# Kernel optimization log

Hardware: AMD Instinct MI355X
Metric: run time of the kernel (lower is better)

The kernel has to match this reference:

```python
import jax, jax.numpy as jnp
import numpy as np

B, S, HID = 32, 577, 768
NH, HD = 12, 64  # num heads, head dim (HID = NH*HD)


def setup_inputs() -> dict:
    key = jax.random.key(0)
    ks = jax.random.split(key, 8)
    scale = 1.0 / np.sqrt(HID)
    return {
        "hidden_states": jax.random.normal(ks[0], (B, S, HID), jnp.float32),
        "lateral_states": jax.random.normal(ks[1], (B, NH, S, HD), jnp.float32),
        "Wq": jax.random.normal(ks[2], (HID, HID), jnp.float32) * scale,
        "bq": jax.random.normal(ks[3], (HID,), jnp.float32) * 0.02,
        "Wk": jax.random.normal(ks[4], (HID, HID), jnp.float32) * scale,
        "bk": jax.random.normal(ks[5], (HID,), jnp.float32) * 0.02,
        "Wv": jax.random.normal(ks[6], (HID, HID), jnp.float32) * scale,
        "bv": jax.random.normal(ks[7], (HID,), jnp.float32) * 0.02,
        "mix_with": 0,  # 0 -> 'q', 1 -> 'k', 2 -> 'v'
    }


def _heads(x):
    # [B, S, HID] -> [B, NH, S, HD]
    return x.reshape(B, S, NH, HD).transpose(0, 2, 1, 3)


def reference(hidden_states, lateral_states, Wq, bq, Wk, bk, Wv, bv, mix_with):
    q = _heads(hidden_states @ Wq.T + bq)
    k = _heads(hidden_states @ Wk.T + bk)
    v = _heads(hidden_states @ Wv.T + bv)
    if mix_with == 0:
        q = q * lateral_states
    elif mix_with == 1:
        k = k * lateral_states
    elif mix_with == 2:
        v = v * lateral_states
    else:
        raise ValueError("mix_with must be 0 (q), 1 (k), or 2 (v)")
    scores = jnp.einsum("bhqd,bhkd->bhqk", q, k) / jnp.sqrt(jnp.float32(HD))
    probs = jax.nn.softmax(scores, axis=-1)
    ctx = jnp.einsum("bhqk,bhkd->bhqd", probs, v)
    # [B, NH, S, HD] -> [B, S, HID]
    return ctx.transpose(0, 2, 1, 3).reshape(B, S, HID)
```

## Files before the change

### kernel.cpp

```cpp
#include <hip/hip_runtime.h>

#define B_    32
#define S_    577
#define HID_  768
#define NH_   12
#define HD_   64
#define SPAD  640
#define SB_   5
#define MT_   160
#define KT_   12
#define NT_   18

typedef __attribute__((ext_vector_type(8))) short short8;
typedef __attribute__((ext_vector_type(4))) short short4s;
typedef __attribute__((ext_vector_type(4))) float float4_;

static __device__ __forceinline__ float bf2f(short s) {
    union { float f; unsigned u; } cvt;
    cvt.u = ((unsigned)(unsigned short)s) << 16;
    return cvt.f;
}
static __device__ __forceinline__ short f2bf(float f) {
    union { float f; unsigned u; } cvt;
    cvt.f = f;
    unsigned u = cvt.u;
    unsigned r = u + 0x7FFF + ((u >> 16) & 1);
    return (short)(r >> 16);
}

__global__ __launch_bounds__(256) void convA_kernel(
    const float* __restrict__ X, short* __restrict__ ximg)
{
    const int mt = blockIdx.x, kt = blockIdx.y;
    const int b = mt / SB_, sb = mt - b * SB_;
    short* img = ximg + ((size_t)mt * KT_ + kt) * 8192;
#pragma unroll
    for (int i = 0; i < 4; ++i) {
        const int j = i * 256 + threadIdx.x;
        const int row = j >> 3, kg = j & 7;
        const int s = sb * 128 + row;
        const int srow = (s < S_) ? s : 0;
        const float* src = X + ((size_t)b * S_ + srow) * HID_ + kt * 64 + kg * 8;
        float4_ f0 = *(const float4_*)src;
        float4_ f1 = *(const float4_*)(src + 4);
        short8 s8;
#pragma unroll
        for (int e = 0; e < 4; ++e) { s8[e] = f2bf(f0[e]); s8[e + 4] = f2bf(f1[e]); }
        *(short8*)(img + ((size_t)kg * 128 + row) * 8) = s8;
    }
}

__global__ __launch_bounds__(256) void convB_kernel(
    const float* __restrict__ Wq, const float* __restrict__ Wk,
    const float* __restrict__ Wv, short* __restrict__ wimg)
{
    const int nt = blockIdx.x, kt = blockIdx.y;
    const int z = nt / 6;
    const float* W = (z == 0) ? Wq : (z == 1) ? Wk : Wv;
    const int n0 = (nt - z * 6) * 128;
    short* img = wimg + ((size_t)nt * KT_ + kt) * 8192;
#pragma unroll
    for (int i = 0; i < 4; ++i) {
        const int j = i * 256 + threadIdx.x;
        const int row = j >> 3, kg = j & 7;
        const float* src = W + (size_t)(n0 + row) * HID_ + kt * 64 + kg * 8;
        float4_ f0 = *(const float4_*)src;
        float4_ f1 = *(const float4_*)(src + 4);
        short8 s8;
#pragma unroll
        for (int e = 0; e < 4; ++e) { s8[e] = f2bf(f0[e]); s8[e + 4] = f2bf(f1[e]); }
        *(short8*)(img + ((size_t)kg * 128 + row) * 8) = s8;
    }
}

__global__ __launch_bounds__(256) void gemm_kernel(
    const short* __restrict__ ximg, const short* __restrict__ wimg,
    const float* __restrict__ bq, const float* __restrict__ bk,
    const float* __restrict__ bv,
    const float* __restrict__ lat, const int* __restrict__ mixw,
    short* __restrict__ qo, short* __restrict__ ko, short* __restrict__ vo)
{
    __shared__ __align__(16) short eP[4][4608];

    const int bid0 = blockIdx.x;
    const int bids = (bid0 & 7) * 360 + (bid0 >> 3);
    const int mt = bids / NT_;
    const int nt = bids - mt * NT_;

    const int z   = nt / 6;
    const int nz0 = (nt - z * 6) * 128;
    const int b   = mt / SB_;
    const int s0  = (mt - b * SB_) * 128;

    const int tid  = threadIdx.x;
    const int wave = tid >> 6;
    const int lane = tid & 63;
    const int quad = lane >> 4;
    const int l16  = lane & 15;

    const short* ag = ximg + ((size_t)mt * KT_) * 8192;
    const short* bg = wimg + ((size_t)nt * KT_) * 8192;

    float4_ acc[4][4] = {};
    const int r0 = (wave & 1) * 64 + l16;
    const int c0 = (wave >> 1) * 64 + l16;

    for (int kt = 0; kt < KT_; ++kt) {
        const short* ak = ag + (size_t)kt * 8192;
        const short* bk8p = bg + (size_t)kt * 8192;
#pragma unroll
        for (int c = 0; c < 2; ++c) {
            const int kb = (c * 4 + quad) * 128;
            short8 af[4], bf4[4];
#pragma unroll
            for (int mi = 0; mi < 4; ++mi)
                af[mi] = *(const short8*)(ak + (kb + r0 + mi * 16) * 8);
#pragma unroll
            for (int g = 0; g < 4; ++g)
                bf4[g] = *(const short8*)(bk8p + (kb + c0 + g * 16) * 8);
            __builtin_amdgcn_s_setprio(1);
#pragma unroll
            for (int mi = 0; mi < 4; ++mi)
#pragma unroll
                for (int g = 0; g < 4; ++g)
                    acc[mi][g] = __builtin_amdgcn_mfma_f32_16x16x32_bf16(
                        af[mi], bf4[g], acc[mi][g], 0, 0, 0);
            __builtin_amdgcn_s_setprio(0);
        }
    }

    const int mwv = *mixw;
    const float* bb = (z == 0) ? bq : (z == 1) ? bk : bv;
    const int hh   = (nz0 + (wave >> 1) * 64) >> 6;
    const size_t bh = (size_t)b * NH_ + hh;
    const int sW   = s0 + (wave & 1) * 64;
    const int ch   = sW >> 6;
    short* P = eP[wave];

    if (z < 2) {
#pragma unroll
        for (int mi = 0; mi < 4; ++mi)
#pragma unroll
            for (int i = 0; i < 4; ++i) {
                const int ml = mi * 16 + quad * 4 + i;
                const int s  = sW + ml;
                const float* lp =
                    lat + (bh * S_ + (s < S_ ? s : S_ - 1)) * HD_;
#pragma unroll
                for (int g = 0; g < 4; ++g) {
                    const int d = g * 16 + l16;
                    float val = acc[mi][g][i] + bb[hh * 64 + d];
                    if (z == mwv) val *= lp[d];
                    P[ml * 72 + d] = f2bf(val);
                }
            }
    } else {
#pragma unroll
        for (int mi = 0; mi < 4; ++mi)
#pragma unroll
            for (int g = 0; g < 4; ++g) {
                const int d  = g * 16 + l16;
                const int mb = mi * 16 + quad * 4;
                short4s w;
#pragma unroll
                for (int i = 0; i < 4; ++i) {
                    const int s = sW + mb + i;
                    float val = acc[mi][g][i] + bb[hh * 64 + d];
                    if (mwv == 2)
                        val *= lat[(bh * S_ + (s < S_ ? s : S_ - 1)) * HD_ + d];
                    w[i] = f2bf(val);
                }
                *(short4s*)(P + d * 72 + mb) = w;
            }
    }

    const int rr = lane >> 3, cc = lane & 7;
    if (z == 0) {
        short* qb = qo + (size_t)bh * SPAD * HD_;
#pragma unroll
        for (int j = 0; j < 8; ++j) {
            const int r = j * 8 + rr;
            *(short8*)(qb + (size_t)(sW + r) * 64 + cc * 8) =
                *(const short8*)(P + r * 72 + cc * 8);
        }
    } else if (z == 1) {
        short* kb = ko + ((size_t)bh * 10 + ch) * 4096;
#pragma unroll
        for (int j = 0; j < 8; ++j) {
            const int r = j * 8 + rr;
            *(short8*)(kb + (cc * 64 + r) * 8) =
                *(const short8*)(P + r * 72 + cc * 8);
        }
    } else {
        short* vb = vo + ((size_t)bh * 10 + ch) * 4096;
#pragma unroll
        for (int j = 0; j < 8; ++j) {
            const int r = j * 8 + rr;
            *(short8*)(vb + (cc * 64 + r) * 8) =
                *(const short8*)(P + r * 72 + cc * 8);
        }
    }
}

__global__ __launch_bounds__(256) void attn_kernel(
    const short* __restrict__ q, const short* __restrict__ k,
    const short* __restrict__ vt, float* __restrict__ out)
{
    __shared__ __align__(16) short pbuf[4][16][64];

    const int bid0 = blockIdx.x;
    const int bids = (bid0 & 7) * 480 + (bid0 >> 3);
    const int bh = bids / 10;
    const int qt = bids - bh * 10;

    const int b    = bh / NH_;
    const int h    = bh - b * NH_;
    const int tid  = threadIdx.x;
    const int wave = tid >> 6;
    const int lane = tid & 63;
    const int quad = lane >> 4;
    const int l16  = lane & 15;
    const int q0   = qt * 64 + wave * 16;

    const short* qp   = q  + (size_t)bh * SPAD * HD_;
    const short* kimg = k  + (size_t)bh * 40960;
    const short* vimg = vt + (size_t)bh * 40960;

    const short8 aq0 = *(const short8*)(qp + (size_t)(q0 + l16) * HD_ + quad * 8);
    const short8 aq1 = *(const short8*)(qp + (size_t)(q0 + l16) * HD_ + 32 + quad * 8);

    float m_i[4], l_i[4];
    float4_ O[4] = {};
#pragma unroll
    for (int i = 0; i < 4; ++i) { m_i[i] = -3.0e38f; l_i[i] = 0.0f; }

    for (int kc = 0; kc < 10; ++kc) {
        const int key0 = kc * 64;
        const short* Kc = kimg + (size_t)kc * 4096;
        const short* Vc = vimg + (size_t)kc * 4096;

        float4_ sc[4] = {};
#pragma unroll
        for (int c = 0; c < 2; ++c) {
            const int kb = (c * 4 + quad) * 64;
            const short8 aq = c ? aq1 : aq0;
            short8 bk8[4];
#pragma unroll
            for (int g = 0; g < 4; ++g)
                bk8[g] = *(const short8*)(Kc + (kb + g * 16 + l16) * 8);
            __builtin_amdgcn_s_setprio(1);
#pragma unroll
            for (int g = 0; g < 4; ++g)
                sc[g] = __builtin_amdgcn_mfma_f32_16x16x32_bf16(aq, bk8[g], sc[g], 0, 0, 0);
            __builtin_amdgcn_s_setprio(0);
        }

        float kmask[4];
#pragma unroll
        for (int g = 0; g < 4; ++g)
            kmask[g] = (key0 + g * 16 + l16 < S_) ? 0.0f : -3.0e38f;

        float alpha[4];
#pragma unroll
        for (int i = 0; i < 4; ++i) {
            float s0 = sc[0][i] * 0.125f + kmask[0];
            float s1 = sc[1][i] * 0.125f + kmask[1];
            float s2 = sc[2][i] * 0.125f + kmask[2];
            float s3 = sc[3][i] * 0.125f + kmask[3];
            float cm = fmaxf(fmaxf(s0, s1), fmaxf(s2, s3));
#pragma unroll
            for (int off = 1; off < 16; off <<= 1)
                cm = fmaxf(cm, __shfl_xor(cm, off));
            const float mn = fmaxf(m_i[i], cm);
            alpha[i] = __expf(m_i[i] - mn);
            m_i[i] = mn;
            const short p0 = f2bf(__expf(s0 - mn));
            const short p1 = f2bf(__expf(s1 - mn));
            const short p2 = f2bf(__expf(s2 - mn));
            const short p3 = f2bf(__expf(s3 - mn));
            pbuf[wave][quad * 4 + i][l16]      = p0;
            pbuf[wave][quad * 4 + i][l16 + 16] = p1;
            pbuf[wave][quad * 4 + i][l16 + 32] = p2;
            pbuf[wave][quad * 4 + i][l16 + 48] = p3;
            float rs = (bf2f(p0) + bf2f(p1)) + (bf2f(p2) + bf2f(p3));
#pragma unroll
            for (int off = 1; off < 16; off <<= 1)
                rs += __shfl_xor(rs, off);
            l_i[i] = l_i[i] * alpha[i] + rs;
        }

#pragma unroll
        for (int g = 0; g < 4; ++g)
#pragma unroll
            for (int i = 0; i < 4; ++i) O[g][i] *= alpha[i];

#pragma unroll
        for (int c = 0; c < 2; ++c) {
            const short8 ap = *(const short8*)(&pbuf[wave][l16][c * 32 + quad * 8]);
            const int kb = (c * 4 + quad) * 64;
            short8 bv8[4];
#pragma unroll
            for (int g = 0; g < 4; ++g)
                bv8[g] = *(const short8*)(Vc + (kb + g * 16 + l16) * 8);
            __builtin_amdgcn_s_setprio(1);
#pragma unroll
            for (int g = 0; g < 4; ++g)
                O[g] = __builtin_amdgcn_mfma_f32_16x16x32_bf16(ap, bv8[g], O[g], 0, 0, 0);
            __builtin_amdgcn_s_setprio(0);
        }
    }

#pragma unroll
    for (int i = 0; i < 4; ++i) {
        const int s = q0 + quad * 4 + i;
        if (s >= S_) continue;
        const float inv = 1.0f / l_i[i];
#pragma unroll
        for (int g = 0; g < 4; ++g)
            out[((size_t)b * S_ + s) * HID_ + h * HD_ + g * 16 + l16] = O[g][i] * inv;
    }
}

extern "C" void kernel_launch(void* const* d_in, const int* in_sizes, int n_in,
                              void* d_out, int out_size, void* d_ws, size_t ws_size,
                              hipStream_t stream) {
    (void)in_sizes; (void)n_in; (void)out_size; (void)ws_size;

    const float* X   = (const float*)d_in[0];
    const float* lat = (const float*)d_in[1];
    const float* Wq  = (const float*)d_in[2];
    const float* bq  = (const float*)d_in[3];
    const float* Wk  = (const float*)d_in[4];
    const float* bk  = (const float*)d_in[5];
    const float* Wv  = (const float*)d_in[6];
    const float* bv  = (const float*)d_in[7];
    const int* mixw  = (const int*)d_in[8];
    float* out = (float*)d_out;

    const size_t per = (size_t)B_ * NH_ * SPAD * HD_;
    short* qw   = (short*)d_ws;
    short* kw   = qw + per;
    short* vw   = kw + per;
    short* wimg = vw + per;
    short* ximg = wimg + (size_t)NT_ * KT_ * 8192;

    convA_kernel<<<dim3(MT_, KT_), 256, 0, stream>>>(X, ximg);
    convB_kernel<<<dim3(NT_, KT_), 256, 0, stream>>>(Wq, Wk, Wv, wimg);
    gemm_kernel<<<dim3(NT_ * MT_), 256, 0, stream>>>(
        ximg, wimg, bq, bk, bv, lat, mixw, qw, kw, vw);
    attn_kernel<<<dim3(3840), 256, 0, stream>>>(qw, kw, vw, out);
}
```

Before: 406.5 us.

## Double per-block tile sizes in projection GEMM and attention kernels

The projection GEMM now has each block compute a 128x256 output tile, with each wave owning 64x128 and 32 accumulators, so A fragments are reused across twice as many columns. The attention kernel has each wave handle 32 query rows instead of 16, so every K and V fragment load feeds two MFMA row tiles. Grid sizes are halved to match. Both changes cut global and cache traffic per FLOP, but raise register pressure, which may lower occupancy, and leave fewer blocks for load balance.

```diff
diff --git a/kernel.cpp b/kernel.cpp
--- a/kernel.cpp
+++ b/kernel.cpp
@@ -83,12 +83,12 @@
     __shared__ __align__(16) short eP[4][4608];
 
     const int bid0 = blockIdx.x;
-    const int bids = (bid0 & 7) * 360 + (bid0 >> 3);
-    const int mt = bids / NT_;
-    const int nt = bids - mt * NT_;
-
-    const int z   = nt / 6;
-    const int nz0 = (nt - z * 6) * 128;
+    const int bids = (bid0 & 7) * 180 + (bid0 >> 3);
+    const int mt  = bids / 9;
+    const int nt9 = bids - mt * 9;
+
+    const int z   = nt9 / 3;
+    const int nb0 = (nt9 - z * 3) * 256;
     const int b   = mt / SB_;
     const int s0  = (mt - b * SB_) * 128;
 
@@ -97,13 +97,14 @@
     const int lane = tid & 63;
     const int quad = lane >> 4;
     const int l16  = lane & 15;
-
-    const short* ag = ximg + ((size_t)mt * KT_) * 8192;
-    const short* bg = wimg + ((size_t)nt * KT_) * 8192;
-
-    float4_ acc[4][4] = {};
-    const int r0 = (wave & 1) * 64 + l16;
-    const int c0 = (wave >> 1) * 64 + l16;
+    const int wr   = wave & 1;
+    const int wc   = wave >> 1;
+
+    const short* ag = ximg + (size_t)mt * KT_ * 8192;
+    const short* bg = wimg + (size_t)(z * 6 + (nb0 >> 7) + wc) * KT_ * 8192;
+
+    float4_ acc[4][8] = {};
+    const int r0 = wr * 64 + l16;
 
     for (int kt = 0; kt < KT_; ++kt) {
         const short* ak = ag + (size_t)kt * 8192;
@@ -111,93 +112,97 @@
 #pragma unroll
         for (int c = 0; c < 2; ++c) {
             const int kb = (c * 4 + quad) * 128;
-            short8 af[4], bf4[4];
+            short8 af[4], bf[8];
 #pragma unroll
             for (int mi = 0; mi < 4; ++mi)
                 af[mi] = *(const short8*)(ak + (kb + r0 + mi * 16) * 8);
 #pragma unroll
-            for (int g = 0; g < 4; ++g)
-                bf4[g] = *(const short8*)(bk8p + (kb + c0 + g * 16) * 8);
+            for (int g = 0; g < 8; ++g)
+                bf[g] = *(const short8*)(bk8p + (kb + g * 16 + l16) * 8);
             __builtin_amdgcn_s_setprio(1);
 #pragma unroll
             for (int mi = 0; mi < 4; ++mi)
 #pragma unroll
-                for (int g = 0; g < 4; ++g)
+                for (int g = 0; g < 8; ++g)
                     acc[mi][g] = __builtin_amdgcn_mfma_f32_16x16x32_bf16(
-                        af[mi], bf4[g], acc[mi][g], 0, 0, 0);
+                        af[mi], bf[g], acc[mi][g], 0, 0, 0);
             __builtin_amdgcn_s_setprio(0);
         }
     }
 
     const int mwv = *mixw;
     const float* bb = (z == 0) ? bq : (z == 1) ? bk : bv;
-    const int hh   = (nz0 + (wave >> 1) * 64) >> 6;
-    const size_t bh = (size_t)b * NH_ + hh;
-    const int sW   = s0 + (wave & 1) * 64;
-    const int ch   = sW >> 6;
+    const int sW = s0 + wr * 64;
+    const int ch = sW >> 6;
     short* P = eP[wave];
-
-    if (z < 2) {
-#pragma unroll
-        for (int mi = 0; mi < 4; ++mi)
-#pragma unroll
-            for (int i = 0; i < 4; ++i) {
-                const int ml = mi * 16 + quad * 4 + i;
-                const int s  = sW + ml;
-                const float* lp =
-                    lat + (bh * S_ + (s < S_ ? s : S_ - 1)) * HD_;
-#pragma unroll
-                for (int g = 0; g < 4; ++g) {
-                    const int d = g * 16 + l16;
-                    float val = acc[mi][g][i] + bb[hh * 64 + d];
-                    if (z == mwv) val *= lp[d];
-                    P[ml * 72 + d] = f2bf(val);
+    const int rr = lane >> 3, cc = lane & 7;
+
+#pragma unroll
+    for (int hs = 0; hs < 2; ++hs) {
+        const int hh = (nb0 >> 6) + wc * 2 + hs;
+        const size_t bh = (size_t)b * NH_ + hh;
+
+        if (z < 2) {
+#pragma unroll
+            for (int mi = 0; mi < 4; ++mi)
+#pragma unroll
+                for (int i = 0; i < 4; ++i) {
+                    const int ml = mi * 16 + quad * 4 + i;
+                    const int s  = sW + ml;
+                    const float* lp =
+                        lat + (bh * S_ + (s < S_ ? s : S_ - 1)) * HD_;
+#pragma unroll
+                    for (int gg = 0; gg < 4; ++gg) {
+                        const int d = gg * 16 + l16;
+                        float val = acc[mi][hs * 4 + gg][i] + bb[hh * 64 + d];
+                        if (z == mwv) val *= lp[d];
+                        P[ml * 72 + d] = f2bf(val);
+                    }
                 }
-            }
-    } else {
-#pragma unroll
-        for (int mi = 0; mi < 4; ++mi)
-#pragma unroll
-            for (int g = 0; g < 4; ++g) {
-                const int d  = g * 16 + l16;
-                const int mb = mi * 16 + quad * 4;
-                short4s w;
-#pragma unroll
-                for (int i = 0; i < 4; ++i) {
-                    const int s = sW + mb + i;
-                    float val = acc[mi][g][i] + bb[hh * 64 + d];
-                    if (mwv == 2)
-                        val *= lat[(bh * S_ + (s < S_ ? s : S_ - 1)) * HD_ + d];
-                    w[i] = f2bf(val);
+        } else {
+#pragma unroll
+            for (int mi = 0; mi < 4; ++mi)
+#pragma unroll
+                for (int gg = 0; gg < 4; ++gg) {
+                    const int d  = gg * 16 + l16;
+                    const int mb = mi * 16 + quad * 4;
+                    short4s w;
+#pragma unroll
+                    for (int i = 0; i < 4; ++i) {
+                        const int s = sW + mb + i;
+                        float val = acc[mi][hs * 4 + gg][i] + bb[hh * 64 + d];
+                        if (mwv == 2)
+                            val *= lat[(bh * S_ + (s < S_ ? s : S_ - 1)) * HD_ + d];
+                        w[i] = f2bf(val);
+                    }
+                    *(short4s*)(P + d * 72 + mb) = w;
                 }
-                *(short4s*)(P + d * 72 + mb) = w;
-            }
-    }
-
-    const int rr = lane >> 3, cc = lane & 7;
-    if (z == 0) {
-        short* qb = qo + (size_t)bh * SPAD * HD_;
-#pragma unroll
-        for (int j = 0; j < 8; ++j) {
-            const int r = j * 8 + rr;
-            *(short8*)(qb + (size_t)(sW + r) * 64 + cc * 8) =
-                *(const short8*)(P + r * 72 + cc * 8);
-        }
-    } else if (z == 1) {
-        short* kb = ko + ((size_t)bh * 10 + ch) * 4096;
-#pragma unroll
-        for (int j = 0; j < 8; ++j) {
-            const int r = j * 8 + rr;
-            *(short8*)(kb + (cc * 64 + r) * 8) =
-                *(const short8*)(P + r * 72 + cc * 8);
-        }
-    } else {
-        short* vb = vo + ((size_t)bh * 10 + ch) * 4096;
-#pragma unroll
-        for (int j = 0; j < 8; ++j) {
-            const int r = j * 8 + rr;
-            *(short8*)(vb + (cc * 64 + r) * 8) =
-                *(const short8*)(P + r * 72 + cc * 8);
+        }
+
+        if (z == 0) {
+            short* qb = qo + (size_t)bh * SPAD * HD_;
+#pragma unroll
+            for (int j = 0; j < 8; ++j) {
+                const int r = j * 8 + rr;
+                *(short8*)(qb + (size_t)(sW + r) * 64 + cc * 8) =
+                    *(const short8*)(P + r * 72 + cc * 8);
+            }
+        } else if (z == 1) {
+            short* kb_ = ko + ((size_t)bh * 10 + ch) * 4096;
+#pragma unroll
+            for (int j = 0; j < 8; ++j) {
+                const int r = j * 8 + rr;
+                *(short8*)(kb_ + (cc * 64 + r) * 8) =
+                    *(const short8*)(P + r * 72 + cc * 8);
+            }
+        } else {
+            short* vb = vo + ((size_t)bh * 10 + ch) * 4096;
+#pragma unroll
+            for (int j = 0; j < 8; ++j) {
+                const int r = j * 8 + rr;
+                *(short8*)(vb + (cc * 64 + r) * 8) =
+                    *(const short8*)(P + r * 72 + cc * 8);
+            }
         }
     }
 }
@@ -206,12 +211,12 @@
     const short* __restrict__ q, const short* __restrict__ k,
     const short* __restrict__ vt, float* __restrict__ out)
 {
-    __shared__ __align__(16) short pbuf[4][16][64];
+    __shared__ __align__(16) short pbuf[4][2][16][64];
 
     const int bid0 = blockIdx.x;
-    const int bids = (bid0 & 7) * 480 + (bid0 >> 3);
-    const int bh = bids / 10;
-    const int qt = bids - bh * 10;
+    const int bids = (bid0 & 7) * 240 + (bid0 >> 3);
+    const int bh = bids / 5;
+    const int qt = bids - bh * 5;
 
     const int b    = bh / NH_;
     const int h    = bh - b * NH_;
@@ -220,38 +225,47 @@
     const int lane = tid & 63;
     const int quad = lane >> 4;
     const int l16  = lane & 15;
-    const int q0   = qt * 64 + wave * 16;
+    const int q0   = qt * 128 + wave * 32;
 
     const short* qp   = q  + (size_t)bh * SPAD * HD_;
     const short* kimg = k  + (size_t)bh * 40960;
     const short* vimg = vt + (size_t)bh * 40960;
 
-    const short8 aq0 = *(const short8*)(qp + (size_t)(q0 + l16) * HD_ + quad * 8);
-    const short8 aq1 = *(const short8*)(qp + (size_t)(q0 + l16) * HD_ + 32 + quad * 8);
-
-    float m_i[4], l_i[4];
-    float4_ O[4] = {};
-#pragma unroll
-    for (int i = 0; i < 4; ++i) { m_i[i] = -3.0e38f; l_i[i] = 0.0f; }
+    short8 aq[2][2];
+#pragma unroll
+    for (int t = 0; t < 2; ++t)
+#pragma unroll
+        for (int c = 0; c < 2; ++c)
+            aq[t][c] = *(const short8*)(qp + (size_t)(q0 + t * 16 + l16) * HD_
+                                        + c * 32 + quad * 8);
+
+    float m_i[2][4], l_i[2][4];
+    float4_ O[2][4] = {};
+#pragma unroll
+    for (int t = 0; t < 2; ++t)
+#pragma unroll
+        for (int i = 0; i < 4; ++i) { m_i[t][i] = -3.0e38f; l_i[t][i] = 0.0f; }
 
     for (int kc = 0; kc < 10; ++kc) {
         const int key0 = kc * 64;
         const short* Kc = kimg + (size_t)kc * 4096;
         const short* Vc = vimg + (size_t)kc * 4096;
 
-        float4_ sc[4] = {};
+        float4_ sc[2][4] = {};
 #pragma unroll
         for (int c = 0; c < 2; ++c) {
             const int kb = (c * 4 + quad) * 64;
-            const short8 aq = c ? aq1 : aq0;
             short8 bk8[4];
 #pragma unroll
             for (int g = 0; g < 4; ++g)
                 bk8[g] = *(const short8*)(Kc + (kb + g * 16 + l16) * 8);
             __builtin_amdgcn_s_setprio(1);
 #pragma unroll
-            for (int g = 0; g < 4; ++g)
-                sc[g] = __builtin_amdgcn_mfma_f32_16x16x32_bf16(aq, bk8[g], sc[g], 0, 0, 0);
+            for (int t = 0; t < 2; ++t)
+#pragma unroll
+                for (int g = 0; g < 4; ++g)
+                    sc[t][g] = __builtin_amdgcn_mfma_f32_16x16x32_bf16(
+                        aq[t][c], bk8[g], sc[t][g], 0, 0, 0);
             __builtin_amdgcn_s_setprio(0);
         }
 
@@ -260,43 +274,46 @@
         for (int g = 0; g < 4; ++g)
             kmask[g] = (key0 + g * 16 + l16 < S_) ? 0.0f : -3.0e38f;
 
-        float alpha[4];
-#pragma unroll
-        for (int i = 0; i < 4; ++i) {
-            float s0 = sc[0][i] * 0.125f + kmask[0];
-            float s1 = sc[1][i] * 0.125f + kmask[1];
-            float s2 = sc[2][i] * 0.125f + kmask[2];
-            float s3 = sc[3][i] * 0.125f + kmask[3];
-            float cm = fmaxf(fmaxf(s0, s1), fmaxf(s2, s3));
-#pragma unroll
-            for (int off = 1; off < 16; off <<= 1)
-                cm = fmaxf(cm, __shfl_xor(cm, off));
-            const float mn = fmaxf(m_i[i], cm);
-            alpha[i] = __expf(m_i[i] - mn);
-            m_i[i] = mn;
-            const short p0 = f2bf(__expf(s0 - mn));
-            const short p1 = f2bf(__expf(s1 - mn));
-            const short p2 = f2bf(__expf(s2 - mn));
-            const short p3 = f2bf(__expf(s3 - mn));
-            pbuf[wave][quad * 4 + i][l16]      = p0;
-            pbuf[wave][quad * 4 + i][l16 + 16] = p1;
-            pbuf[wave][quad * 4 + i][l16 + 32] = p2;
-            pbuf[wave][quad * 4 + i][l16 + 48] = p3;
-            float rs = (bf2f(p0) + bf2f(p1)) + (bf2f(p2) + bf2f(p3));
-#pragma unroll
-            for (int off = 1; off < 16; off <<= 1)
-                rs += __shfl_xor(rs, off);
-            l_i[i] = l_i[i] * alpha[i] + rs;
-        }
-
-#pragma unroll
-        for (int g = 0; g < 4; ++g)
-#pragma unroll
-            for (int i = 0; i < 4; ++i) O[g][i] *= alpha[i];
+        float alpha[2][4];
+#pragma unroll
+        for (int t = 0; t < 2; ++t)
+#pragma unroll
+            for (int i = 0; i < 4; ++i) {
+                float s0 = sc[t][0][i] * 0.125f + kmask[0];
+                float s1 = sc[t][1][i] * 0.125f + kmask[1];
+                float s2 = sc[t][2][i] * 0.125f + kmask[2];
+                float s3 = sc[t][3][i] * 0.125f + kmask[3];
+                float cm = fmaxf(fmaxf(s0, s1), fmaxf(s2, s3));
+#pragma unroll
+                for (int off = 1; off < 16; off <<= 1)
+                    cm = fmaxf(cm, __shfl_xor(cm, off));
+                const float mn = fmaxf(m_i[t][i], cm);
+                alpha[t][i] = __expf(m_i[t][i] - mn);
+                m_i[t][i] = mn;
+                const short p0 = f2bf(__expf(s0 - mn));
+                const short p1 = f2bf(__expf(s1 - mn));
+                const short p2 = f2bf(__expf(s2 - mn));
+                const short p3 = f2bf(__expf(s3 - mn));
+                pbuf[wave][t][quad * 4 + i][l16]      = p0;
+                pbuf[wave][t][quad * 4 + i][l16 + 16] = p1;
+                pbuf[wave][t][quad * 4 + i][l16 + 32] = p2;
+                pbuf[wave][t][quad * 4 + i][l16 + 48] = p3;
+                float rs = (bf2f(p0) + bf2f(p1)) + (bf2f(p2) + bf2f(p3));
+#pragma unroll
+                for (int off = 1; off < 16; off <<= 1)
+                    rs += __shfl_xor(rs, off);
+                l_i[t][i] = l_i[t][i] * alpha[t][i] + rs;
+            }
+
+#pragma unroll
+        for (int t = 0; t < 2; ++t)
+#pragma unroll
+            for (int g = 0; g < 4; ++g)
+#pragma unroll
+                for (int i = 0; i < 4; ++i) O[t][g][i] *= alpha[t][i];
 
 #pragma unroll
         for (int c = 0; c < 2; ++c) {
-            const short8 ap = *(const short8*)(&pbuf[wave][l16][c * 32 + quad * 8]);
             const int kb = (c * 4 + quad) * 64;
             short8 bv8[4];
 #pragma unroll
@@ -304,21 +321,30 @@
                 bv8[g] = *(const short8*)(Vc + (kb + g * 16 + l16) * 8);
             __builtin_amdgcn_s_setprio(1);
 #pragma unroll
+            for (int t = 0; t < 2; ++t) {
+                const short8 ap =
+                    *(const short8*)(&pbuf[wave][t][l16][c * 32 + quad * 8]);
+#pragma unroll
+                for (int g = 0; g < 4; ++g)
+                    O[t][g] = __builtin_amdgcn_mfma_f32_16x16x32_bf16(
+                        ap, bv8[g], O[t][g], 0, 0, 0);
+            }
+            __builtin_amdgcn_s_setprio(0);
+        }
+    }
+
+#pragma unroll
+    for (int t = 0; t < 2; ++t)
+#pragma unroll
+        for (int i = 0; i < 4; ++i) {
+            const int s = q0 + t * 16 + quad * 4 + i;
+            if (s >= S_) continue;
+            const float inv = 1.0f / l_i[t][i];
+#pragma unroll
             for (int g = 0; g < 4; ++g)
-                O[g] = __builtin_amdgcn_mfma_f32_16x16x32_bf16(ap, bv8[g], O[g], 0, 0, 0);
-            __builtin_amdgcn_s_setprio(0);
-        }
-    }
-
-#pragma unroll
-    for (int i = 0; i < 4; ++i) {
-        const int s = q0 + quad * 4 + i;
-        if (s >= S_) continue;
-        const float inv = 1.0f / l_i[i];
-#pragma unroll
-        for (int g = 0; g < 4; ++g)
-            out[((size_t)b * S_ + s) * HID_ + h * HD_ + g * 16 + l16] = O[g][i] * inv;
-    }
+                out[((size_t)b * S_ + s) * HID_ + h * HD_ + g * 16 + l16] =
+                    O[t][g][i] * inv;
+        }
 }
 
 extern "C" void kernel_launch(void* const* d_in, const int* in_sizes, int n_in,
@@ -346,7 +372,7 @@
 
     convA_kernel<<<dim3(MT_, KT_), 256, 0, stream>>>(X, ximg);
     convB_kernel<<<dim3(NT_, KT_), 256, 0, stream>>>(Wq, Wk, Wv, wimg);
-    gemm_kernel<<<dim3(NT_ * MT_), 256, 0, stream>>>(
+    gemm_kernel<<<dim3(1440), 256, 0, stream>>>(
         ximg, wimg, bq, bk, bv, lat, mixw, qw, kw, vw);
-    attn_kernel<<<dim3(3840), 256, 0, stream>>>(qw, kw, vw, out);
-}
+    attn_kernel<<<dim3(1920), 256, 0, stream>>>(qw, kw, vw, out);
+}
```

Measured after the change: 550.7 us. 35.5% more time.

## Transpose QK^T MFMA so each lane owns one query row in softmax

Applied to the files above, without the earlier changes.

Swaps the MFMA operands for the score product so each lane holds all scores of a single query row. This cuts the per-row max and sum reductions from four 16-lane shuffle trees to two cross-quad shuffles, and it folds the 1/sqrt(d) scale into one FMA before the exponential. The probability tile is written to shared memory with an XOR swizzle to avoid bank conflicts, and the key mask is only applied on the last chunk. Alpha and the final normalisers are redistributed back to the output layout with shuffles, which adds a few cross-lane operations in return.

```diff
diff --git a/kernel.cpp b/kernel.cpp
--- a/kernel.cpp
+++ b/kernel.cpp
@@ -184,11 +184,11 @@
                 *(const short8*)(P + r * 72 + cc * 8);
         }
     } else if (z == 1) {
-        short* kb = ko + ((size_t)bh * 10 + ch) * 4096;
+        short* kb_ = ko + ((size_t)bh * 10 + ch) * 4096;
 #pragma unroll
         for (int j = 0; j < 8; ++j) {
             const int r = j * 8 + rr;
-            *(short8*)(kb + (cc * 64 + r) * 8) =
+            *(short8*)(kb_ + (cc * 64 + r) * 8) =
                 *(const short8*)(P + r * 72 + cc * 8);
         }
     } else {
@@ -229,13 +229,13 @@
     const short8 aq0 = *(const short8*)(qp + (size_t)(q0 + l16) * HD_ + quad * 8);
     const short8 aq1 = *(const short8*)(qp + (size_t)(q0 + l16) * HD_ + 32 + quad * 8);
 
-    float m_i[4], l_i[4];
+    float m_i = -3.0e38f, l_i = 0.0f;
     float4_ O[4] = {};
-#pragma unroll
-    for (int i = 0; i < 4; ++i) { m_i[i] = -3.0e38f; l_i[i] = 0.0f; }
+
+    char* pw = (char*)&pbuf[wave][l16][0];
+    const int swz = (l16 & 7) << 4;
 
     for (int kc = 0; kc < 10; ++kc) {
-        const int key0 = kc * 64;
         const short* Kc = kimg + (size_t)kc * 4096;
         const short* Vc = vimg + (size_t)kc * 4096;
 
@@ -244,80 +244,93 @@
         for (int c = 0; c < 2; ++c) {
             const int kb = (c * 4 + quad) * 64;
             const short8 aq = c ? aq1 : aq0;
-            short8 bk8[4];
-#pragma unroll
-            for (int g = 0; g < 4; ++g)
-                bk8[g] = *(const short8*)(Kc + (kb + g * 16 + l16) * 8);
+            short8 kf[4];
+#pragma unroll
+            for (int g = 0; g < 4; ++g)
+                kf[g] = *(const short8*)(Kc + (kb + g * 16 + l16) * 8);
             __builtin_amdgcn_s_setprio(1);
 #pragma unroll
             for (int g = 0; g < 4; ++g)
-                sc[g] = __builtin_amdgcn_mfma_f32_16x16x32_bf16(aq, bk8[g], sc[g], 0, 0, 0);
+                sc[g] = __builtin_amdgcn_mfma_f32_16x16x32_bf16(kf[g], aq, sc[g], 0, 0, 0);
             __builtin_amdgcn_s_setprio(0);
         }
 
-        float kmask[4];
+        if (kc == 9) {
+#pragma unroll
+            for (int g = 0; g < 4; ++g)
+#pragma unroll
+                for (int i = 0; i < 4; ++i)
+                    if (576 + g * 16 + quad * 4 + i >= S_) sc[g][i] = -3.0e38f;
+        }
+
+        float cm = sc[0][0];
 #pragma unroll
         for (int g = 0; g < 4; ++g)
-            kmask[g] = (key0 + g * 16 + l16 < S_) ? 0.0f : -3.0e38f;
-
-        float alpha[4];
-#pragma unroll
-        for (int i = 0; i < 4; ++i) {
-            float s0 = sc[0][i] * 0.125f + kmask[0];
-            float s1 = sc[1][i] * 0.125f + kmask[1];
-            float s2 = sc[2][i] * 0.125f + kmask[2];
-            float s3 = sc[3][i] * 0.125f + kmask[3];
-            float cm = fmaxf(fmaxf(s0, s1), fmaxf(s2, s3));
-#pragma unroll
-            for (int off = 1; off < 16; off <<= 1)
-                cm = fmaxf(cm, __shfl_xor(cm, off));
-            const float mn = fmaxf(m_i[i], cm);
-            alpha[i] = __expf(m_i[i] - mn);
-            m_i[i] = mn;
-            const short p0 = f2bf(__expf(s0 - mn));
-            const short p1 = f2bf(__expf(s1 - mn));
-            const short p2 = f2bf(__expf(s2 - mn));
-            const short p3 = f2bf(__expf(s3 - mn));
-            pbuf[wave][quad * 4 + i][l16]      = p0;
-            pbuf[wave][quad * 4 + i][l16 + 16] = p1;
-            pbuf[wave][quad * 4 + i][l16 + 32] = p2;
-            pbuf[wave][quad * 4 + i][l16 + 48] = p3;
-            float rs = (bf2f(p0) + bf2f(p1)) + (bf2f(p2) + bf2f(p3));
-#pragma unroll
-            for (int off = 1; off < 16; off <<= 1)
-                rs += __shfl_xor(rs, off);
-            l_i[i] = l_i[i] * alpha[i] + rs;
-        }
-
+#pragma unroll
+            for (int i = 0; i < 4; ++i) cm = fmaxf(cm, sc[g][i]);
+        cm = fmaxf(cm, __shfl_xor(cm, 16));
+        cm = fmaxf(cm, __shfl_xor(cm, 32));
+
+        const float mn    = fmaxf(m_i, cm);
+        const float alpha = __expf((m_i - mn) * 0.125f);
+        m_i = mn;
+        const float mo = mn * 0.125f;
+
+        float rs = 0.0f;
+#pragma unroll
+        for (int g = 0; g < 4; ++g) {
+            short4s w;
+#pragma unroll
+            for (int i = 0; i < 4; ++i) {
+                const float p = __expf(__builtin_fmaf(sc[g][i], 0.125f, -mo));
+                const short pb = f2bf(p);
+                w[i] = pb;
+                rs += bf2f(pb);
+            }
+            *(short4s*)(pw + ((g * 32 + quad * 8) ^ swz)) = w;
+        }
+        rs += __shfl_xor(rs, 16);
+        rs += __shfl_xor(rs, 32);
+        l_i = l_i * alpha + rs;
+
+        float av[4];
+#pragma unroll
+        for (int i = 0; i < 4; ++i)
+            av[i] = __shfl(alpha, quad * 20 + i);
 #pragma unroll
         for (int g = 0; g < 4; ++g)
 #pragma unroll
-            for (int i = 0; i < 4; ++i) O[g][i] *= alpha[i];
+            for (int i = 0; i < 4; ++i) O[g][i] *= av[i];
 
 #pragma unroll
         for (int c = 0; c < 2; ++c) {
-            const short8 ap = *(const short8*)(&pbuf[wave][l16][c * 32 + quad * 8]);
+            const short8 ap =
+                *(const short8*)(pw + ((c * 64 + quad * 16) ^ swz));
             const int kb = (c * 4 + quad) * 64;
-            short8 bv8[4];
-#pragma unroll
-            for (int g = 0; g < 4; ++g)
-                bv8[g] = *(const short8*)(Vc + (kb + g * 16 + l16) * 8);
+            short8 vf[4];
+#pragma unroll
+            for (int g = 0; g < 4; ++g)
+                vf[g] = *(const short8*)(Vc + (kb + g * 16 + l16) * 8);
             __builtin_amdgcn_s_setprio(1);
 #pragma unroll
             for (int g = 0; g < 4; ++g)
-                O[g] = __builtin_amdgcn_mfma_f32_16x16x32_bf16(ap, bv8[g], O[g], 0, 0, 0);
+                O[g] = __builtin_amdgcn_mfma_f32_16x16x32_bf16(ap, vf[g], O[g], 0, 0, 0);
             __builtin_amdgcn_s_setprio(0);
         }
     }
 
+    float linv[4];
+#pragma unroll
+    for (int i = 0; i < 4; ++i)
+        linv[i] = 1.0f / __shfl(l_i, quad * 20 + i);
 #pragma unroll
     for (int i = 0; i < 4; ++i) {
         const int s = q0 + quad * 4 + i;
         if (s >= S_) continue;
-        const float inv = 1.0f / l_i[i];
 #pragma unroll
         for (int g = 0; g < 4; ++g)
-            out[((size_t)b * S_ + s) * HID_ + h * HD_ + g * 16 + l16] = O[g][i] * inv;
+            out[((size_t)b * S_ + s) * HID_ + h * HD_ + g * 16 + l16] =
+                O[g][i] * linv[i];
     }
 }
 
@@ -346,7 +359,7 @@
 
     convA_kernel<<<dim3(MT_, KT_), 256, 0, stream>>>(X, ximg);
     convB_kernel<<<dim3(NT_, KT_), 256, 0, stream>>>(Wq, Wk, Wv, wimg);
-    gemm_kernel<<<dim3(NT_ * MT_), 256, 0, stream>>>(
+    gemm_kernel<<<dim3(2880), 256, 0, stream>>>(
         ximg, wimg, bq, bk, bv, lat, mixw, qw, kw, vw);
     attn_kernel<<<dim3(3840), 256, 0, stream>>>(qw, kw, vw, out);
 }
```

Measured after the change: 386.9 us. 1.05x faster.
